# Optimization experiments

Hardware: AMD Instinct MI355X
Metric: run time of the kernel (lower is better)

The kernel has to match this reference:

```python
import jax, jax.numpy as jnp
import numpy as np
from jax.scipy.special import erf

DIM = 8  # Cl(3,0) multivector dimension
BV_IDX = jnp.array([3, 5, 6])  # blades with popcount==2 in bitmask ordering
GRADES = np.array([bin(i).count('1') for i in range(DIM)])
GRADES_J = jnp.asarray(GRADES)
REV_SIGN = jnp.asarray(np.where((GRADES * (GRADES - 1) // 2) % 2 == 0, 1.0, -1.0).astype(np.float32))


def _cayley():
    # Geometric-product structure tensor for Cl(3,0): (e_a e_b) = sign * e_{a^b}
    C = np.zeros((DIM, DIM, DIM), dtype=np.float32)
    for a in range(DIM):
        for b in range(DIM):
            s, t = 0, a >> 1
            while t:
                s += bin(t & b).count('1')
                t >>= 1
            C[a, b, a ^ b] = -1.0 if (s & 1) else 1.0
    return jnp.asarray(C)

CAYLEY = _cayley()


def rotor_exp(bv):
    # bv: [..., 3] bivector coefficients -> rotor multivector [..., 8]
    # B^2 = -|B|^2 in Cl(3,0), so exp(B) = cos|B| + sin|B|/|B| * B
    theta = jnp.sqrt(jnp.sum(bv * bv, axis=-1, keepdims=True))
    sinc = jnp.where(theta > 1e-6, jnp.sin(theta) / jnp.maximum(theta, 1e-6), 1.0)
    R = jnp.zeros(bv.shape[:-1] + (DIM,), bv.dtype)
    R = R.at[..., 0].set(jnp.cos(theta)[..., 0])
    R = R.at[..., BV_IDX].set(sinc * bv)
    return R


def reverse(x):
    return x * REV_SIGN


def setup_inputs() -> dict:
    key = jax.random.key(0)
    ks = jax.random.split(key, 8)
    B, C, A = 65536, 32, 5
    return {
        'state': jax.random.normal(ks[0], (B, C, DIM), jnp.float32),
        'action': jax.random.randint(ks[1], (B,), 0, A),
        'action_bivectors': 0.1 * jax.random.normal(ks[2], (A, 3), jnp.float32),
        'norm_scale': jnp.ones((C,), jnp.float32),
        'rotor_bv': 0.1 * jax.random.normal(ks[3], (C, 3), jnp.float32),
        'lin_W': jax.random.normal(ks[4], (C, C, 4), jnp.float32) / np.sqrt(C),
        'lin_b': jnp.zeros((C,), jnp.float32),
        'reward_W': jax.random.normal(ks[5], (1, C), jnp.float32) / np.sqrt(C),
        'reward_b': jnp.zeros((1,), jnp.float32),
    }


def reference(state, action, action_bivectors, norm_scale, rotor_bv, lin_W, lin_b, reward_W, reward_b):
    # 1-2. gather action bivector, rotor R = exp(-B/2)
    bv = -0.5 * action_bivectors[action]                 # [B, 3]
    R = rotor_exp(bv)                                    # [B, 8]
    Rr = reverse(R)
    # 3. sandwich s' = R s R~ per channel
    t = jnp.einsum('bi,bcj,ijk->bck', R, state, CAYLEY)
    x = jnp.einsum('bck,bl,klm->bcm', t, Rr, CAYLEY)     # [B, C, 8]
    # 4. GA refine block (residual)
    # CliffordLayerNorm: per-channel multivector norm + learnable scale
    n = jnp.sqrt(jnp.sum(x * x, axis=-1, keepdims=True) + 1e-6)
    h = x / n * norm_scale[None, :, None]
    # GeometricGELU: gate whole multivector by Phi(scalar part)
    gate = 0.5 * (1.0 + erf(h[..., :1] * jnp.asarray(0.7071067811865476, h.dtype)))
    h = h * gate
    # RotorLayer: per-channel learned rotor sandwich
    Rc = rotor_exp(-0.5 * rotor_bv)                      # [C, 8]
    Rcr = reverse(Rc)
    t2 = jnp.einsum('ci,bcj,ijk->bck', Rc, h, CAYLEY)
    h = jnp.einsum('bck,cl,klm->bcm', t2, Rcr, CAYLEY)
    # CliffordLinear: grade-wise channel mixing
    Wg = lin_W[:, :, GRADES_J]                           # [C_out, C_in, 8]
    h = jnp.einsum('bid,oid->bod', h, Wg)
    h = h.at[..., 0].add(lin_b)
    next_state = x + h
    # 5. reward from grade-0
    reward = next_state[:, :, 0] @ reward_W.T + reward_b  # [B, 1]
    return reward, next_state
```

## Files before the change

kernel.cpp:

```cpp
#include <hip/hip_runtime.h>
#include <hip/hip_bf16.h>

typedef __bf16 bf16x8 __attribute__((ext_vector_type(8)));
typedef float  floatx4 __attribute__((ext_vector_type(4)));

__device__ __forceinline__ __bf16 to_bf16(float f) {
    unsigned u = __builtin_bit_cast(unsigned, f);
    u += 0x7FFFu + ((u >> 16) & 1u);
    unsigned short h = (unsigned short)(u >> 16);
    return __builtin_bit_cast(__bf16, h);
}

__host__ __device__ constexpr float csign(int a, int b) {
    int s = 0;
    for (int k = 1; k < 4; ++k) {
        int t = (a >> k) & b;
        s += (t & 1) + ((t >> 1) & 1) + ((t >> 2) & 1);
    }
    return (s & 1) ? -1.0f : 1.0f;
}

__device__ __forceinline__ void rotor_sandwich(const float r[4], const float s_in[8], float x[8]) {
    constexpr int RI[4] = {0, 3, 5, 6};
    float t[8];
#pragma unroll
    for (int k = 0; k < 8; ++k) t[k] = 0.f;
#pragma unroll
    for (int ia = 0; ia < 4; ++ia) {
#pragma unroll
        for (int jb = 0; jb < 8; ++jb) {
            t[RI[ia] ^ jb] += csign(RI[ia], jb) * r[ia] * s_in[jb];
        }
    }
    const float rr[4] = {r[0], -r[1], -r[2], -r[3]};
#pragma unroll
    for (int k = 0; k < 8; ++k) x[k] = 0.f;
#pragma unroll
    for (int ka = 0; ka < 8; ++ka) {
#pragma unroll
        for (int ib = 0; ib < 4; ++ib) {
            x[ka ^ RI[ib]] += csign(ka, RI[ib]) * t[ka] * rr[ib];
        }
    }
}

__device__ __forceinline__ void rotor_from_bv(float b0, float b1, float b2, float r[4]) {
    float t2 = b0 * b0 + b1 * b1 + b2 * b2;
    float th = sqrtf(t2);
    float sc = (th > 1e-6f) ? (__sinf(th) / th) : 1.0f;
    r[0] = __cosf(th);
    r[1] = sc * b0;
    r[2] = sc * b1;
    r[3] = sc * b2;
}

__device__ __forceinline__ void channel_fwd(const float r[4], float nsc,
                                            const float* __restrict__ rbv,
                                            float4 s0, float4 s1,
                                            float* xo, float* hf) {
    float s_in[8] = {s0.x, s0.y, s0.z, s0.w, s1.x, s1.y, s1.z, s1.w};
    float xv[8];
    rotor_sandwich(r, s_in, xv);
    float ss = 1e-6f;
#pragma unroll
    for (int d = 0; d < 8; ++d) ss += xv[d] * xv[d];
    float hscale = nsc * rsqrtf(ss);
    float gate = 0.5f * (1.0f + erff(xv[0] * hscale * 0.70710678118654752440f));
    float g2 = hscale * gate;
    float hv[8];
#pragma unroll
    for (int d = 0; d < 8; ++d) hv[d] = xv[d] * g2;
    float rc[4];
    rotor_from_bv(-0.5f * rbv[0], -0.5f * rbv[1], -0.5f * rbv[2], rc);
    rotor_sandwich(rc, hv, hf);
#pragma unroll
    for (int d = 0; d < 8; ++d) xo[d] = xv[d];
}

__global__ __launch_bounds__(256, 2) void dyn_kernel(
    const float* __restrict__ state, const int* __restrict__ action,
    const float* __restrict__ act_bv, const float* __restrict__ norm_scale,
    const float* __restrict__ rotor_bv, const float* __restrict__ lin_W,
    const float* __restrict__ lin_b, const float* __restrict__ reward_W,
    const float* __restrict__ reward_b,
    float* __restrict__ out_reward, float* __restrict__ out_next)
{
    const int tid   = threadIdx.x;
    const int lane  = tid & 63;
    const int wv    = tid >> 6;
    const int bl    = lane & 15;
    const int q     = lane >> 4;
    const int bbase = blockIdx.x * 64 + wv * 16;
    const int b     = bbase + bl;
    const int cbase = 8 * q;

    bf16x8 Wf[4][2];
#pragma unroll
    for (int hh = 0; hh < 2; ++hh) {
        const int o = bl + 16 * hh;
#pragma unroll
        for (int j = 0; j < 8; ++j) {
            float4 w = ((const float4*)lin_W)[o * 32 + cbase + j];
            Wf[0][hh][j] = to_bf16(w.x);
            Wf[1][hh][j] = to_bf16(w.y);
            Wf[2][hh][j] = to_bf16(w.z);
            Wf[3][hh][j] = to_bf16(w.w);
        }
    }
    const float lb[2] = {lin_b[bl], lin_b[bl + 16]};
    const float rwlo = reward_W[bl], rwhi = reward_W[bl + 16];

    float r[4];
    {
        const int a = action[b];
        const float* p = act_bv + a * 3;
        rotor_from_bv(-0.5f * p[0], -0.5f * p[1], -0.5f * p[2], r);
    }

    bf16x8 ah[8];
    bf16x8 ax[8];
    const float* sp = state + ((size_t)b * 32 + cbase) * 8;
#pragma unroll
    for (int i = 0; i < 4; ++i) {
        const int cA = cbase + 2 * i, cB = cA + 1;
        float4 sa0 = ((const float4*)sp)[4 * i + 0];
        float4 sa1 = ((const float4*)sp)[4 * i + 1];
        float4 sb0 = ((const float4*)sp)[4 * i + 2];
        float4 sb1 = ((const float4*)sp)[4 * i + 3];
        float xa[8], ha[8], xb[8], hb[8];
        channel_fwd(r, norm_scale[cA], rotor_bv + cA * 3, sa0, sa1, xa, ha);
        channel_fwd(r, norm_scale[cB], rotor_bv + cB * 3, sb0, sb1, xb, hb);
#pragma unroll
        for (int d = 0; d < 8; ++d) {
            ah[d][2 * i]     = to_bf16(ha[d]);
            ah[d][2 * i + 1] = to_bf16(hb[d]);
            ax[d][2 * i]     = to_bf16(xa[d]);
            ax[d][2 * i + 1] = to_bf16(xb[d]);
        }
    }

    const __bf16 one_bf  = __builtin_bit_cast(__bf16, (unsigned short)0x3F80);
    const __bf16 zero_bf = __builtin_bit_cast(__bf16, (unsigned short)0x0000);
    bf16x8 BI[2];
#pragma unroll
    for (int hh = 0; hh < 2; ++hh)
#pragma unroll
        for (int j = 0; j < 8; ++j)
            BI[hh][j] = (cbase + j == bl + 16 * hh) ? one_bf : zero_bf;

    constexpr int GR[8] = {0, 1, 1, 2, 1, 2, 2, 3};
    floatx4 acc[8][2];
#pragma unroll
    for (int d = 0; d < 8; ++d) {
#pragma unroll
        for (int hh = 0; hh < 2; ++hh) {
            floatx4 c0;
            const float ci = (d == 0) ? lb[hh] : 0.f;
            c0[0] = ci; c0[1] = ci; c0[2] = ci; c0[3] = ci;
            floatx4 t = __builtin_amdgcn_mfma_f32_16x16x32_bf16(ah[d], Wf[GR[d]][hh], c0, 0, 0, 0);
            acc[d][hh] = __builtin_amdgcn_mfma_f32_16x16x32_bf16(ax[d], BI[hh],       t,  0, 0, 0);
        }
    }

#pragma unroll
    for (int hh = 0; hh < 2; ++hh) {
#pragma unroll
        for (int rg = 0; rg < 4; ++rg) {
            float* dst = out_next +
                ((size_t)(bbase + 4 * q + rg) * 32 + (bl + 16 * hh)) * 8;
            float4 v0 = {acc[0][hh][rg], acc[1][hh][rg], acc[2][hh][rg], acc[3][hh][rg]};
            float4 v1 = {acc[4][hh][rg], acc[5][hh][rg], acc[6][hh][rg], acc[7][hh][rg]};
            ((float4*)dst)[0] = v0;
            ((float4*)dst)[1] = v1;
        }
    }

    float r4[4];
#pragma unroll
    for (int rg = 0; rg < 4; ++rg)
        r4[rg] = acc[0][0][rg] * rwlo + acc[0][1][rg] * rwhi;
#pragma unroll
    for (int m = 1; m <= 8; m <<= 1) {
#pragma unroll
        for (int rg = 0; rg < 4; ++rg)
            r4[rg] += __shfl_xor(r4[rg], m, 64);
    }
    if (bl < 4) {
        float v = (bl == 0) ? r4[0] : (bl == 1) ? r4[1] : (bl == 2) ? r4[2] : r4[3];
        out_reward[bbase + 4 * q + bl] = v + reward_b[0];
    }
}

extern "C" void kernel_launch(void* const* d_in, const int* in_sizes, int n_in,
                              void* d_out, int out_size, void* d_ws, size_t ws_size,
                              hipStream_t stream) {
    const float* state      = (const float*)d_in[0];
    const int*   action     = (const int*)  d_in[1];
    const float* act_bv     = (const float*)d_in[2];
    const float* norm_scale = (const float*)d_in[3];
    const float* rotor_bv   = (const float*)d_in[4];
    const float* lin_W      = (const float*)d_in[5];
    const float* lin_b      = (const float*)d_in[6];
    const float* reward_W   = (const float*)d_in[7];
    const float* reward_b   = (const float*)d_in[8];

    float* out = (float*)d_out;
    const int B = in_sizes[1];
    float* out_reward = out;
    float* out_next   = out + B;

    dim3 grid(B / 64), block(256);
    hipLaunchKernelGGL(dyn_kernel, grid, block, 0, stream,
                       state, action, act_bv, norm_scale, rotor_bv,
                       lin_W, lin_b, reward_W, reward_b, out_reward, out_next);
    (void)n_in; (void)out_size; (void)d_ws; (void)ws_size;
}
```

Before: 148.0 us.

## Replace rotor sandwiches with 3x3 rotation matrices and precompute weight tables

Rewrites each rotor sandwich as a 3x3 rotation applied separately to the vector and bivector parts, with scalar and pseudoscalar passing through unchanged. This replaces the full Cayley-table products with a handful of FMAs. A small prologue kernel precomputes the per-channel rotation matrices and the bf16 weight fragments in MFMA layout, so the main kernel no longer reconverts weights or recomputes channel rotors per thread. It also issues all state loads up front and packs bf16 pairs with a perm instruction, which adds a second launch and a global-memory table dependency.

```diff
diff --git a/kernel.cpp b/kernel.cpp
--- a/kernel.cpp
+++ b/kernel.cpp
@@ -3,45 +3,20 @@
 
 typedef __bf16 bf16x8 __attribute__((ext_vector_type(8)));
 typedef float  floatx4 __attribute__((ext_vector_type(4)));
-
-__device__ __forceinline__ __bf16 to_bf16(float f) {
+typedef int    intx4   __attribute__((ext_vector_type(4)));
+
+__device__ __align__(16) float g_Qc[32][12];
+__device__ __align__(16) unsigned short g_Wbf[4 * 2 * 64 * 8];
+
+__device__ __forceinline__ unsigned bf16_bits_rne(float f) {
     unsigned u = __builtin_bit_cast(unsigned, f);
     u += 0x7FFFu + ((u >> 16) & 1u);
-    unsigned short h = (unsigned short)(u >> 16);
-    return __builtin_bit_cast(__bf16, h);
-}
-
-__host__ __device__ constexpr float csign(int a, int b) {
-    int s = 0;
-    for (int k = 1; k < 4; ++k) {
-        int t = (a >> k) & b;
-        s += (t & 1) + ((t >> 1) & 1) + ((t >> 2) & 1);
-    }
-    return (s & 1) ? -1.0f : 1.0f;
-}
-
-__device__ __forceinline__ void rotor_sandwich(const float r[4], const float s_in[8], float x[8]) {
-    constexpr int RI[4] = {0, 3, 5, 6};
-    float t[8];
-#pragma unroll
-    for (int k = 0; k < 8; ++k) t[k] = 0.f;
-#pragma unroll
-    for (int ia = 0; ia < 4; ++ia) {
-#pragma unroll
-        for (int jb = 0; jb < 8; ++jb) {
-            t[RI[ia] ^ jb] += csign(RI[ia], jb) * r[ia] * s_in[jb];
-        }
-    }
-    const float rr[4] = {r[0], -r[1], -r[2], -r[3]};
-#pragma unroll
-    for (int k = 0; k < 8; ++k) x[k] = 0.f;
-#pragma unroll
-    for (int ka = 0; ka < 8; ++ka) {
-#pragma unroll
-        for (int ib = 0; ib < 4; ++ib) {
-            x[ka ^ RI[ib]] += csign(ka, RI[ib]) * t[ka] * rr[ib];
-        }
-    }
+    return u;
+}
+__device__ __forceinline__ int pack2(float lo, float hi) {
+    unsigned ul = __builtin_bit_cast(unsigned, lo) + 0x8000u;
+    unsigned uh = __builtin_bit_cast(unsigned, hi) + 0x8000u;
+    return (int)__builtin_amdgcn_perm(uh, ul, 0x07060302u);
 }
 
 __device__ __forceinline__ void rotor_from_bv(float b0, float b1, float b2, float r[4]) {
@@ -54,33 +29,74 @@
     r[3] = sc * b2;
 }
 
-__device__ __forceinline__ void channel_fwd(const float r[4], float nsc,
-                                            const float* __restrict__ rbv,
-                                            float4 s0, float4 s1,
-                                            float* xo, float* hf) {
-    float s_in[8] = {s0.x, s0.y, s0.z, s0.w, s1.x, s1.y, s1.z, s1.w};
-    float xv[8];
-    rotor_sandwich(r, s_in, xv);
+__device__ __forceinline__ void q_from_rotor(const float r[4], float Q[9]) {
+    const float w = r[0], a = r[1], b = r[2], c = r[3];
+    const float ww = w * w, aa = a * a, bb = b * b, cc = c * c;
+    Q[0] = ww - aa - bb + cc;
+    Q[1] = 2.f * (w * a - b * c);
+    Q[2] = 2.f * (w * b + a * c);
+    Q[3] = -2.f * (w * a + b * c);
+    Q[4] = ww - aa + bb - cc;
+    Q[5] = 2.f * (w * c - a * b);
+    Q[6] = 2.f * (a * c - w * b);
+    Q[7] = -2.f * (w * c + a * b);
+    Q[8] = ww + aa - bb - cc;
+}
+
+__device__ __forceinline__ void qapply(const float Q[9], const float s[8], float o[8]) {
+    o[0] = s[0];
+    o[1] = Q[0] * s[1] + Q[1] * s[2] + Q[2] * s[4];
+    o[2] = Q[3] * s[1] + Q[4] * s[2] + Q[5] * s[4];
+    o[4] = Q[6] * s[1] + Q[7] * s[2] + Q[8] * s[4];
+    o[3] = Q[8] * s[3] - Q[7] * s[5] + Q[6] * s[6];
+    o[5] = -Q[5] * s[3] + Q[4] * s[5] - Q[3] * s[6];
+    o[6] = Q[2] * s[3] - Q[1] * s[5] + Q[0] * s[6];
+    o[7] = s[7];
+}
+
+__device__ __forceinline__ void chan(const float QR[9], const float Qc[9], float nsc,
+                                     float4 s0, float4 s1, float x[8], float hf[8]) {
+    float s[8] = {s0.x, s0.y, s0.z, s0.w, s1.x, s1.y, s1.z, s1.w};
+    qapply(QR, s, x);
     float ss = 1e-6f;
 #pragma unroll
-    for (int d = 0; d < 8; ++d) ss += xv[d] * xv[d];
-    float hscale = nsc * rsqrtf(ss);
-    float gate = 0.5f * (1.0f + erff(xv[0] * hscale * 0.70710678118654752440f));
-    float g2 = hscale * gate;
-    float hv[8];
-#pragma unroll
-    for (int d = 0; d < 8; ++d) hv[d] = xv[d] * g2;
-    float rc[4];
-    rotor_from_bv(-0.5f * rbv[0], -0.5f * rbv[1], -0.5f * rbv[2], rc);
-    rotor_sandwich(rc, hv, hf);
-#pragma unroll
-    for (int d = 0; d < 8; ++d) xo[d] = xv[d];
+    for (int d = 0; d < 8; ++d) ss += x[d] * x[d];
+    const float hs = nsc * rsqrtf(ss);
+    const float gate = 0.5f * (1.0f + erff(x[0] * hs * 0.70710678118654752440f));
+    const float g2 = hs * gate;
+    float y[8];
+    qapply(Qc, x, y);
+#pragma unroll
+    for (int d = 0; d < 8; ++d) hf[d] = y[d] * g2;
+}
+
+__global__ void build_tables(const float* __restrict__ rotor_bv,
+                             const float* __restrict__ lin_W) {
+    const int t = threadIdx.x;
+    if (t < 32) {
+        float r[4];
+        rotor_from_bv(-0.5f * rotor_bv[3 * t], -0.5f * rotor_bv[3 * t + 1],
+                      -0.5f * rotor_bv[3 * t + 2], r);
+        float Q[9];
+        q_from_rotor(r, Q);
+#pragma unroll
+        for (int k = 0; k < 9; ++k) g_Qc[t][k] = Q[k];
+        g_Qc[t][9] = 0.f; g_Qc[t][10] = 0.f; g_Qc[t][11] = 0.f;
+    }
+#pragma unroll
+    for (int i = 0; i < 16; ++i) {
+        const int idx = t * 16 + i;
+        const int j = idx & 7, lane = (idx >> 3) & 63;
+        const int hh = (idx >> 9) & 1, g = idx >> 10;
+        const int bl = lane & 15, q = lane >> 4;
+        g_Wbf[idx] = (unsigned short)(
+            bf16_bits_rne(lin_W[((bl + 16 * hh) * 32 + 8 * q + j) * 4 + g]) >> 16);
+    }
 }
 
 __global__ __launch_bounds__(256, 2) void dyn_kernel(
     const float* __restrict__ state, const int* __restrict__ action,
     const float* __restrict__ act_bv, const float* __restrict__ norm_scale,
-    const float* __restrict__ rotor_bv, const float* __restrict__ lin_W,
     const float* __restrict__ lin_b, const float* __restrict__ reward_W,
     const float* __restrict__ reward_b,
     float* __restrict__ out_reward, float* __restrict__ out_next)
@@ -94,48 +110,53 @@
     const int b     = bbase + bl;
     const int cbase = 8 * q;
 
+    const float* sp = state + ((size_t)b * 32 + cbase) * 8;
+    float4 sv[16];
+#pragma unroll
+    for (int k = 0; k < 16; ++k) sv[k] = ((const float4*)sp)[k];
+
     bf16x8 Wf[4][2];
 #pragma unroll
-    for (int hh = 0; hh < 2; ++hh) {
-        const int o = bl + 16 * hh;
-#pragma unroll
-        for (int j = 0; j < 8; ++j) {
-            float4 w = ((const float4*)lin_W)[o * 32 + cbase + j];
-            Wf[0][hh][j] = to_bf16(w.x);
-            Wf[1][hh][j] = to_bf16(w.y);
-            Wf[2][hh][j] = to_bf16(w.z);
-            Wf[3][hh][j] = to_bf16(w.w);
-        }
-    }
+    for (int g = 0; g < 4; ++g)
+#pragma unroll
+        for (int hh = 0; hh < 2; ++hh)
+            Wf[g][hh] = ((const bf16x8*)g_Wbf)[(g * 2 + hh) * 64 + lane];
+
     const float lb[2] = {lin_b[bl], lin_b[bl + 16]};
-    const float rwlo = reward_W[bl], rwhi = reward_W[bl + 16];
-
-    float r[4];
+    const float rw[2] = {reward_W[bl], reward_W[bl + 16]};
+
+    float QR[9];
     {
         const int a = action[b];
         const float* p = act_bv + a * 3;
+        float r[4];
         rotor_from_bv(-0.5f * p[0], -0.5f * p[1], -0.5f * p[2], r);
-    }
-
-    bf16x8 ah[8];
-    bf16x8 ax[8];
-    const float* sp = state + ((size_t)b * 32 + cbase) * 8;
+        q_from_rotor(r, QR);
+    }
+
+    int ahw[8][4];
+    int axw[8][4];
 #pragma unroll
     for (int i = 0; i < 4; ++i) {
         const int cA = cbase + 2 * i, cB = cA + 1;
-        float4 sa0 = ((const float4*)sp)[4 * i + 0];
-        float4 sa1 = ((const float4*)sp)[4 * i + 1];
-        float4 sb0 = ((const float4*)sp)[4 * i + 2];
-        float4 sb1 = ((const float4*)sp)[4 * i + 3];
+        float QcA[9], QcB[9];
+        {
+            const float4* qa = (const float4*)g_Qc[cA];
+            const float4* qb = (const float4*)g_Qc[cB];
+            float4 a0 = qa[0], a1 = qa[1], a2 = qa[2];
+            float4 b0 = qb[0], b1 = qb[1], b2 = qb[2];
+            QcA[0]=a0.x; QcA[1]=a0.y; QcA[2]=a0.z; QcA[3]=a0.w;
+            QcA[4]=a1.x; QcA[5]=a1.y; QcA[6]=a1.z; QcA[7]=a1.w; QcA[8]=a2.x;
+            QcB[0]=b0.x; QcB[1]=b0.y; QcB[2]=b0.z; QcB[3]=b0.w;
+            QcB[4]=b1.x; QcB[5]=b1.y; QcB[6]=b1.z; QcB[7]=b1.w; QcB[8]=b2.x;
+        }
         float xa[8], ha[8], xb[8], hb[8];
-        channel_fwd(r, norm_scale[cA], rotor_bv + cA * 3, sa0, sa1, xa, ha);
-        channel_fwd(r, norm_scale[cB], rotor_bv + cB * 3, sb0, sb1, xb, hb);
+        chan(QR, QcA, norm_scale[cA], sv[4 * i + 0], sv[4 * i + 1], xa, ha);
+        chan(QR, QcB, norm_scale[cB], sv[4 * i + 2], sv[4 * i + 3], xb, hb);
 #pragma unroll
         for (int d = 0; d < 8; ++d) {
-            ah[d][2 * i]     = to_bf16(ha[d]);
-            ah[d][2 * i + 1] = to_bf16(hb[d]);
-            ax[d][2 * i]     = to_bf16(xa[d]);
-            ax[d][2 * i + 1] = to_bf16(xb[d]);
+            ahw[d][i] = pack2(ha[d], hb[d]);
+            axw[d][i] = pack2(xa[d], xb[d]);
         }
     }
 
@@ -152,13 +173,17 @@
     floatx4 acc[8][2];
 #pragma unroll
     for (int d = 0; d < 8; ++d) {
+        intx4 aw = {ahw[d][0], ahw[d][1], ahw[d][2], ahw[d][3]};
+        intx4 xw = {axw[d][0], axw[d][1], axw[d][2], axw[d][3]};
+        bf16x8 ah = __builtin_bit_cast(bf16x8, aw);
+        bf16x8 ax = __builtin_bit_cast(bf16x8, xw);
 #pragma unroll
         for (int hh = 0; hh < 2; ++hh) {
             floatx4 c0;
             const float ci = (d == 0) ? lb[hh] : 0.f;
             c0[0] = ci; c0[1] = ci; c0[2] = ci; c0[3] = ci;
-            floatx4 t = __builtin_amdgcn_mfma_f32_16x16x32_bf16(ah[d], Wf[GR[d]][hh], c0, 0, 0, 0);
-            acc[d][hh] = __builtin_amdgcn_mfma_f32_16x16x32_bf16(ax[d], BI[hh],       t,  0, 0, 0);
+            floatx4 t = __builtin_amdgcn_mfma_f32_16x16x32_bf16(ah, Wf[GR[d]][hh], c0, 0, 0, 0);
+            acc[d][hh] = __builtin_amdgcn_mfma_f32_16x16x32_bf16(ax, BI[hh],       t,  0, 0, 0);
         }
     }
 
@@ -178,7 +203,7 @@
     float r4[4];
 #pragma unroll
     for (int rg = 0; rg < 4; ++rg)
-        r4[rg] = acc[0][0][rg] * rwlo + acc[0][1][rg] * rwhi;
+        r4[rg] = acc[0][0][rg] * rw[0] + acc[0][1][rg] * rw[1];
 #pragma unroll
     for (int m = 1; m <= 8; m <<= 1) {
 #pragma unroll
@@ -209,9 +234,9 @@
     float* out_reward = out;
     float* out_next   = out + B;
 
-    dim3 grid(B / 64), block(256);
-    hipLaunchKernelGGL(dyn_kernel, grid, block, 0, stream,
-                       state, action, act_bv, norm_scale, rotor_bv,
-                       lin_W, lin_b, reward_W, reward_b, out_reward, out_next);
+    hipLaunchKernelGGL(build_tables, dim3(1), dim3(256), 0, stream, rotor_bv, lin_W);
+    hipLaunchKernelGGL(dyn_kernel, dim3(B / 64), dim3(256), 0, stream,
+                       state, action, act_bv, norm_scale,
+                       lin_b, reward_W, reward_b, out_reward, out_next);
     (void)n_in; (void)out_size; (void)d_ws; (void)ws_size;
 }
```

After: 142.2 us. 1.04x faster.
